# Optimization experiments

Hardware: AMD Instinct MI355X
Metric: run time of the kernel (lower is better)

The kernel has to match this reference:

```python
import jax, jax.numpy as jnp
import numpy as np

B, T, S, D, H, F = 8, 1024, 1024, 512, 8, 2048
LN_EPS = 1e-5


def _layernorm(x, g, b):
    m = jnp.mean(x, axis=-1, keepdims=True)
    v = jnp.mean((x - m) ** 2, axis=-1, keepdims=True)
    return (x - m) / jnp.sqrt(v + LN_EPS) * g + b


def setup_inputs() -> dict:
    key = jax.random.key(0)
    ks = jax.random.split(key, 32)
    p = lambda k, shape: jax.random.normal(k, shape, jnp.float32) * 0.02
    causal = jnp.where(jnp.triu(jnp.ones((T, T), dtype=bool), 1), -1e9, 0.0).astype(jnp.float32)
    return {
        "x": jax.random.normal(ks[0], (B, T, D), jnp.float32),
        "src_padding_mask": jnp.zeros((B, S, 1), jnp.float32),
        "src_subsq_mask": jnp.zeros((S, S), jnp.float32),  # unused by DecoderLayer math
        "tgt_padding_mask": jnp.zeros((B, T, 1), jnp.float32),
        "tgt_subsq_mask": causal,
        "mem_keys": jax.random.normal(ks[1], (B, S, D), jnp.float32),
        "mem_values": jax.random.normal(ks[2], (B, S, D), jnp.float32),
        # self-attention per-head params, stacked over heads (each head is full-D)
        "Wq_self": p(ks[3], (H, D, D)), "bq_self": p(ks[4], (H, D)),
        "Wk_self": p(ks[5], (H, D, D)), "bk_self": p(ks[6], (H, D)),
        "Wv_self": p(ks[7], (H, D, D)), "bv_self": p(ks[8], (H, D)),
        "Wo_self": p(ks[9], (H * D, D)), "bo_self": p(ks[10], (D,)),
        # memory (cross) attention: only Q per head; keys/values come from encoder
        "Wq_mem": p(ks[11], (H, D, D)), "bq_mem": p(ks[12], (H, D)),
        "Wo_mem": p(ks[13], (H * D, D)), "bo_mem": p(ks[14], (D,)),
        # FFN
        "W1": p(ks[15], (D, F)), "b1": p(ks[16], (F,)),
        "W2": p(ks[17], (F, D)), "b2": p(ks[18], (D,)),
        # LayerNorms
        "ln1_g": jnp.ones((D,), jnp.float32), "ln1_b": jnp.zeros((D,), jnp.float32),
        "ln2_g": jnp.ones((D,), jnp.float32), "ln2_b": jnp.zeros((D,), jnp.float32),
        "ln3_g": jnp.ones((D,), jnp.float32), "ln3_b": jnp.zeros((D,), jnp.float32),
    }


def reference(x, src_padding_mask, src_subsq_mask, tgt_padding_mask, tgt_subsq_mask,
              mem_keys, mem_values,
              Wq_self, bq_self, Wk_self, bk_self, Wv_self, bv_self, Wo_self, bo_self,
              Wq_mem, bq_mem, Wo_mem, bo_mem,
              W1, b1, W2, b2,
              ln1_g, ln1_b, ln2_g, ln2_b, ln3_g, ln3_b):
    b, t, d = x.shape
    h = Wq_self.shape[0]
    inv_sqrt_d = 1.0 / (d ** 0.5)

    # ---- multi-head self-attention (each head full d_model) ----
    q = jnp.einsum('btd,hde->bhte', x, Wq_self) + bq_self[None, :, None, :]
    k = jnp.einsum('btd,hde->bhte', x, Wk_self) + bk_self[None, :, None, :]
    v = jnp.einsum('btd,hde->bhte', x, Wv_self) + bv_self[None, :, None, :]
    att = jnp.einsum('bhte,bhse->bhts', q, k) * inv_sqrt_d
    att = att + tgt_padding_mask.transpose(0, 2, 1)[:, None, :, :]  # [B,1,1,T]
    att = att + tgt_subsq_mask[None, None, :, :]                     # [1,1,T,T]
    a = jax.nn.softmax(att, axis=-1)
    ho = jnp.einsum('bhts,bhse->bhte', a, v)
    cat = ho.transpose(0, 2, 1, 3).reshape(b, t, h * d)  # matches torch.cat head order
    sa = cat @ Wo_self + bo_self
    x1 = _layernorm(sa + x, ln1_g, ln1_b)  # dropout is identity at eval

    # ---- multi-head memory (cross) attention; keys/values shared across heads ----
    qm = jnp.einsum('btd,hde->bhte', x1, Wq_mem) + bq_mem[None, :, None, :]
    attm = jnp.einsum('bhte,bse->bhts', qm, mem_keys) * inv_sqrt_d
    attm = attm + src_padding_mask.transpose(0, 2, 1)[:, None, :, :]
    am = jax.nn.softmax(attm, axis=-1)
    hom = jnp.einsum('bhts,bse->bhte', am, mem_values)
    catm = hom.transpose(0, 2, 1, 3).reshape(b, t, h * d)
    ma = catm @ Wo_mem + bo_mem
    x2 = _layernorm(ma + x1, ln2_g, ln2_b)

    # ---- FFN ----
    ff = jax.nn.relu(x2 @ W1 + b1) @ W2 + b2
    out = _layernorm(ff + x2, ln3_g, ln3_b)
    return out
```

## Files before the change

### kernel.cpp

```cpp
#include <hip/hip_runtime.h>
#include <hip/hip_bf16.h>
#include <cstdint>

#define DEV __device__ __forceinline__

typedef __bf16 bf16_t;
typedef bf16_t bf16x8 __attribute__((ext_vector_type(8)));
typedef float  f32x4  __attribute__((ext_vector_type(4)));

static constexpr int B_ = 8, T_ = 1024, S_ = 1024, D_ = 512, H_ = 8, F_ = 2048;

typedef const __attribute__((address_space(1))) void* gas_ptr;
typedef __attribute__((address_space(3))) void* las_ptr;

DEV void gload_lds16(const void* g, void* l) {
  __builtin_amdgcn_global_load_lds((gas_ptr)g, (las_ptr)l, 16, 0, 0);
}

template<typename OutT, int EPI, int MI, int NI>
__global__ __launch_bounds__(256, (MI == 2 && NI == 2) ? 5 : 2) void gemm_bt(
    const bf16_t* __restrict__ A,  int64_t aH, int64_t aB, int lda,
    const bf16_t* __restrict__ BT, int64_t bH, int64_t bB, int ldb,
    OutT* __restrict__ C,          int64_t cH, int64_t cB, int ldo,
    int K, int ZB,
    const float* __restrict__ bias, int64_t biasH, int64_t biasB,
    float scale,
    const float* __restrict__ pad, int64_t padB,
    const float* __restrict__ subsq, int subsq_ld, int causal,
    int initC, int kcap)
{
  constexpr int BM = MI * 32;
  constexpr int BN = NI * 32;
  constexpr int BNT = NI * 32;

  const unsigned gx = gridDim.x, gy = gridDim.y;
  const unsigned nwg = gx * gy * gridDim.z;
  const unsigned orig = (blockIdx.z * gy + blockIdx.y) * gx + blockIdx.x;
  const unsigned q8 = nwg >> 3, r8 = nwg & 7;
  const unsigned xcd = orig & 7, cidx = orig >> 3;
  const unsigned swz = (xcd < r8 ? xcd * (q8 + 1)
                                 : r8 * (q8 + 1) + (xcd - r8) * q8) + cidx;
  const unsigned bz = swz / (gx * gy);
  const unsigned rm = swz - bz * gx * gy;
  const unsigned by = rm / gx;
  const unsigned bx = rm - by * gx;

  const int z  = bz;
  const int zh = z / ZB, zb = z - zh * ZB;
  A  += zh * aH + zb * aB;
  BT += zh * bH + zb * bB;
  C  += zh * cH + zb * cB;
  const int m0 = by * BM;
  const int n0 = bx * BNT;

  const bool skip = (EPI == 2) && causal && (n0 >= m0 + BM);
  if (skip && causal == 2) return;

  __shared__ __align__(16) bf16_t As[2][BM * 64];
  __shared__ __align__(16) bf16_t Bs[2][BNT * 64];

  const int tid  = threadIdx.x;
  const int lane = tid & 63;
  const int wr   = tid >> 7;
  const int wc   = (tid >> 6) & 1;

  f32x4 acc[MI][NI] = {};

  int Klim = K;
  if (kcap) { const int lim = m0 + BM; Klim = lim < K ? lim : K; }

  auto stage = [&](int buf, int kb) {
    #pragma unroll
    for (int i = 0; i < MI; ++i) {
      const int c = i * 256 + tid;
      const int row = c >> 3;
      const int col = (((c & 7) ^ (row & 7)) << 3);
      gload_lds16(A + (int64_t)(m0 + row) * lda + kb + col, &As[buf][c * 8]);
    }
    #pragma unroll
    for (int i = 0; i < NI; ++i) {
      const int c = i * 256 + tid;
      const int row = c >> 3;
      const int col = (((c & 7) ^ (row & 7)) << 3);
      gload_lds16(BT + (int64_t)(n0 + row) * ldb + kb + col, &Bs[buf][c * 8]);
    }
  };

  if (!skip) {
    const int NT = Klim >> 6;
    stage(0, 0);
    if (NT > 1) stage(1, 64);
    const int hi = lane >> 4, r7 = lane & 7;
    for (int t = 0; t < NT; ++t) {
      if (t + 1 < NT) {
        if constexpr (MI + NI == 4)      asm volatile("s_waitcnt vmcnt(4)" ::: "memory");
        else if constexpr (MI + NI == 6) asm volatile("s_waitcnt vmcnt(6)" ::: "memory");
        else                             asm volatile("s_waitcnt vmcnt(8)" ::: "memory");
      } else {
        asm volatile("s_waitcnt vmcnt(0)" ::: "memory");
      }
      __builtin_amdgcn_s_barrier();
      __builtin_amdgcn_sched_barrier(0);
      const int cur = t & 1;
      bf16x8 af[MI][2], bq[NI][2];
      #pragma unroll
      for (int ks = 0; ks < 2; ++ks) {
        #pragma unroll
        for (int i = 0; i < MI; ++i)
          af[i][ks] = *(const bf16x8*)&As[cur][(wr * (MI * 16) + i * 16 + (lane & 15)) * 64 + (((ks * 4 + hi) ^ r7) << 3)];
        #pragma unroll
        for (int i = 0; i < NI; ++i)
          bq[i][ks] = *(const bf16x8*)&Bs[cur][(wc * (NI * 16) + i * 16 + (lane & 15)) * 64 + (((ks * 4 + hi) ^ r7) << 3)];
      }
      asm volatile("s_waitcnt lgkmcnt(0)" ::: "memory");
      __builtin_amdgcn_sched_barrier(0);
      __builtin_amdgcn_s_barrier();
      if (t + 2 < NT) stage(cur, (t + 2) << 6);
      __builtin_amdgcn_sched_barrier(0);
      __builtin_amdgcn_s_setprio(1);
      #pragma unroll
      for (int ks = 0; ks < 2; ++ks)
        #pragma unroll
        for (int mi = 0; mi < MI; ++mi)
          #pragma unroll
          for (int ni = 0; ni < NI; ++ni)
            acc[mi][ni] = __builtin_amdgcn_mfma_f32_16x16x32_bf16(af[mi][ks], bq[ni][ks], acc[mi][ni], 0, 0, 0);
      __builtin_amdgcn_s_setprio(0);
    }
  }

  const float* bz_ = (EPI != 2 && bias) ? bias + zh * biasH + zb * biasB : nullptr;
  const float* pz  = (EPI == 2 && pad)  ? pad + zb * padB : nullptr;
  #pragma unroll
  for (int ni = 0; ni < NI; ++ni) {
    const int col = n0 + wc * (NI * 16) + ni * 16 + (lane & 15);
    const float badd = bz_ ? bz_[col] : 0.f;
    const float pv   = pz ? pz[col] : 0.f;
    #pragma unroll
    for (int mi = 0; mi < MI; ++mi) {
      const int rowb = m0 + wr * (MI * 16) + mi * 16 + ((lane >> 4) << 2);
      #pragma unroll
      for (int r = 0; r < 4; ++r) {
        const int row = rowb + r;
        const int64_t idx = (int64_t)row * ldo + col;
        float v = acc[mi][ni][r];
        if (EPI == 2) {
          if (skip) v = -1e9f;
          else {
            v = v * scale + pv;
            if (subsq) v += subsq[(int64_t)row * subsq_ld + col];
          }
        } else if (EPI == 3) {
          v += initC ? badd : (float)C[idx];
        } else {
          v += badd;
          if (EPI == 1) v = fmaxf(v, 0.f);
        }
        if constexpr (sizeof(OutT) == 2) C[idx] = (OutT)v;
        else                             C[idx] = v;
      }
    }
  }
  (void)BN;
}

template<int CAUSAL>
__global__ __launch_bounds__(256) void softmax1024b(bf16_t* __restrict__ P)
{
  const int64_t row = blockIdx.x;
  const int len = CAUSAL ? (int)(row % T_) + 1 : 1024;
  const int tid = threadIdx.x;
  const int j4 = tid << 2;
  float v0 = -3e38f, v1 = -3e38f, v2 = -3e38f, v3 = -3e38f;
  if (j4 < len) {
    union { bf16_t b[4]; uint2 u; } in;
    in.u = ((const uint2*)(P + row * 1024))[tid];
    v0 = (float)in.b[0];
    if (j4 + 1 < len) v1 = (float)in.b[1];
    if (j4 + 2 < len) v2 = (float)in.b[2];
    if (j4 + 3 < len) v3 = (float)in.b[3];
  }
  float m = fmaxf(fmaxf(v0, v1), fmaxf(v2, v3));
  #pragma unroll
  for (int off = 32; off; off >>= 1) m = fmaxf(m, __shfl_xor(m, off));
  __shared__ float red[8];
  if ((tid & 63) == 0) red[tid >> 6] = m;
  __syncthreads();
  m = fmaxf(fmaxf(red[0], red[1]), fmaxf(red[2], red[3]));
  const float e0 = (j4     < len) ? __expf(v0 - m) : 0.f;
  const float e1 = (j4 + 1 < len) ? __expf(v1 - m) : 0.f;
  const float e2 = (j4 + 2 < len) ? __expf(v2 - m) : 0.f;
  const float e3 = (j4 + 3 < len) ? __expf(v3 - m) : 0.f;
  float s = e0 + e1 + e2 + e3;
  #pragma unroll
  for (int off = 32; off; off >>= 1) s += __shfl_xor(s, off);
  if ((tid & 63) == 0) red[4 + (tid >> 6)] = s;
  __syncthreads();
  const float inv = 1.f / (red[4] + red[5] + red[6] + red[7]);
  const int lenc = CAUSAL ? ((len + 63) & ~63) : 1024;
  if (j4 < lenc) {
    union { bf16_t b[4]; uint2 u; } o;
    o.b[0] = (bf16_t)(e0 * inv); o.b[1] = (bf16_t)(e1 * inv);
    o.b[2] = (bf16_t)(e2 * inv); o.b[3] = (bf16_t)(e3 * inv);
    ((uint2*)(P + row * 1024))[tid] = o.u;
  }
}

__global__ __launch_bounds__(128) void add_ln512(
    const float* __restrict__ a, const float* __restrict__ r,
    const float* __restrict__ g, const float* __restrict__ be,
    float* __restrict__ yf, bf16_t* __restrict__ yb)
{
  const int64_t row = blockIdx.x;
  const int tid = threadIdx.x;
  const float4 va = ((const float4*)(a + row * 512))[tid];
  const float4 vr = ((const float4*)(r + row * 512))[tid];
  const float x0 = va.x + vr.x, x1 = va.y + vr.y, x2 = va.z + vr.z, x3 = va.w + vr.w;
  float s = x0 + x1 + x2 + x3;
  float q = x0 * x0 + x1 * x1 + x2 * x2 + x3 * x3;
  #pragma unroll
  for (int off = 32; off; off >>= 1) { s += __shfl_xor(s, off); q += __shfl_xor(q, off); }
  __shared__ float red[4];
  if ((tid & 63) == 0) { red[tid >> 6] = s; red[2 + (tid >> 6)] = q; }
  __syncthreads();
  s = red[0] + red[1]; q = red[2] + red[3];
  const float mean = s * (1.f / 512.f);
  const float var  = q * (1.f / 512.f) - mean * mean;
  const float rstd = rsqrtf(var + 1e-5f);
  const float4 g4 = ((const float4*)g)[tid];
  const float4 b4 = ((const float4*)be)[tid];
  const float y0 = (x0 - mean) * rstd * g4.x + b4.x;
  const float y1 = (x1 - mean) * rstd * g4.y + b4.y;
// ... 79 lines not shown
  float* outf = (float*)d_out;

  constexpr int64_t BTD = (int64_t)B_ * T_ * D_;
  constexpr int64_t BTS = (int64_t)B_ * T_ * S_;
  constexpr int64_t DD  = (int64_t)D_ * D_;
  const int M8 = B_ * T_;

  char* p = (char*)d_ws;
  auto alloc = [&](int64_t bytes) -> void* {
    char* r = p; p += (bytes + 255) & ~(int64_t)255; return (void*)r;
  };
  bf16_t* WTqkv = (bf16_t*)alloc(3 * H_ * DD * 2);
  bf16_t* WoT   = (bf16_t*)alloc((int64_t)D_ * H_ * D_ * 2);
  bf16_t* WqmT  = (bf16_t*)alloc(H_ * DD * 2);
  bf16_t* WomT  = (bf16_t*)alloc((int64_t)D_ * H_ * D_ * 2);
  bf16_t* W1T   = (bf16_t*)alloc((int64_t)F_ * D_ * 2);
  bf16_t* W2T   = (bf16_t*)alloc((int64_t)D_ * F_ * 2);
  float*  bqkv  = (float*)alloc(3 * H_ * D_ * 4);
  bf16_t* actb  = (bf16_t*)alloc(BTD * 2);
  bf16_t* mkb   = (bf16_t*)alloc(BTD * 2);
  bf16_t* mvT   = (bf16_t*)alloc(BTD * 2);
  float*  x1f   = (float*)alloc(BTD * 4);

  const int64_t remain = (int64_t)ws_size - (int64_t)(p - (char*)d_ws);
  const int64_t perG   = 3 * BTD * 2 + BTD * 2 + BTS * 2;
  const int64_t hoCat  = (int64_t)B_ * T_ * H_ * D_ * 2;
  int G = 0;
  for (int g = 8; g >= 1; g >>= 1)
    if (remain >= hoCat + (int64_t)g * perG + (4 << 20)) { G = g; break; }
  const int64_t needB = 3 * BTD * 2 + BTD * 2 + BTS * 2 + BTD * 2 + (1 << 20);
  if (G == 0 && remain < needB) return;

  const float scale = 1.0f / sqrtf((float)D_);
  dim3 blk(256);

  castf2b<<<dim3((unsigned)(BTD / 4 / 256)), blk, 0, stream>>>(x, actb, (int)(BTD / 4));
  castf2b<<<dim3((unsigned)(BTD / 4 / 256)), blk, 0, stream>>>(mk, mkb, (int)(BTD / 4));
  tcast<float><<<dim3(D_ / 32, S_ / 32, B_), blk, 0, stream>>>(mv, mvT, S_, D_);
  tcast<float><<<dim3(D_ / 32, D_ / 32, H_), blk, 0, stream>>>(Wq, WTqkv, D_, D_);
  tcast<float><<<dim3(D_ / 32, D_ / 32, H_), blk, 0, stream>>>(Wk, WTqkv + H_ * DD, D_, D_);
  tcast<float><<<dim3(D_ / 32, D_ / 32, H_), blk, 0, stream>>>(Wv, WTqkv + 2 * H_ * DD, D_, D_);
  tcast<float><<<dim3(D_ / 32, (H_ * D_) / 32, 1), blk, 0, stream>>>(Wo, WoT, H_ * D_, D_);
  tcast<float><<<dim3(D_ / 32, D_ / 32, H_), blk, 0, stream>>>(Wqm, WqmT, D_, D_);
  tcast<float><<<dim3(D_ / 32, (H_ * D_) / 32, 1), blk, 0, stream>>>(Wom, WomT, H_ * D_, D_);
  tcast<float><<<dim3(F_ / 32, D_ / 32, 1), blk, 0, stream>>>(W1, W1T, D_, F_);
  tcast<float><<<dim3(D_ / 32, F_ / 32, 1), blk, 0, stream>>>(W2, W2T, F_, D_);
  pack3<<<dim3((H_ * D_ + 255) / 256), blk, 0, stream>>>(bq, bk, bv, bqkv, H_ * D_);

  bf16_t* ffh = nullptr;

  if (G > 0) {
    bf16_t* hoAll = (bf16_t*)alloc(hoCat);
    bf16_t* qkv   = (bf16_t*)alloc(3 * G * BTD * 2);
    bf16_t* vt    = (bf16_t*)alloc((int64_t)G * BTD * 2);
    bf16_t* logit = (bf16_t*)alloc((int64_t)G * BTS * 2);
    ffh = qkv;

    for (int h0 = 0; h0 < H_; h0 += G) {
      gemm_bt<bf16_t, 0, 2, 2><<<dim3(D_ / 64, M8 / 64, 3 * G), blk, 0, stream>>>(
          actb, 0, 0, D_,
          WTqkv + (int64_t)h0 * DD, (int64_t)H_ * DD, DD, D_,
          qkv, (int64_t)G * BTD, BTD, D_,
          D_, G,
          bqkv + h0 * D_, (int64_t)H_ * D_, D_,
          1.f, nullptr, 0, nullptr, 0, 0, 0, 0);
      tcast<bf16_t><<<dim3(D_ / 32, T_ / 32, G * B_), blk, 0, stream>>>(
          qkv + (int64_t)2 * G * BTD, vt, T_, D_);
      gemm_bt<bf16_t, 2, 2, 2><<<dim3(S_ / 64, T_ / 64, G * B_), blk, 0, stream>>>(
          qkv, BTD, (int64_t)T_ * D_, D_,
          qkv + (int64_t)G * BTD, BTD, (int64_t)T_ * D_, D_,
          logit, BTS, (int64_t)T_ * S_, S_,
          D_, B_,
          nullptr, 0, 0,
          scale, tgt_pad, T_, tgt_sub, S_, 2, 0, 0);
      softmax1024b<1><<<dim3((unsigned)(G * B_ * T_)), blk, 0, stream>>>(logit);
      gemm_bt<bf16_t, 0, 2, 2><<<dim3(D_ / 64, T_ / 64, G * B_), blk, 0, stream>>>(
          logit, BTS, (int64_t)T_ * S_, S_,
          vt, (int64_t)B_ * D_ * T_, (int64_t)D_ * T_, T_,
          hoAll + (int64_t)h0 * D_, D_, (int64_t)T_ * H_ * D_, H_ * D_,
          S_, B_,
          nullptr, 0, 0, 1.f, nullptr, 0, nullptr, 0, 0, 0, 1);
    }
    gemm_bt<float, 0, 2, 2><<<dim3(D_ / 64, M8 / 64, 1), blk, 0, stream>>>(
        hoAll, 0, 0, H_ * D_, WoT, 0, 0, H_ * D_, outf, 0, 0, D_,
        H_ * D_, 1, bo, 0, 0, 1.f, nullptr, 0, nullptr, 0, 0, 0, 0);
    add_ln512<<<dim3(M8), dim3(128), 0, stream>>>(outf, x, g1, be1, x1f, actb);

    for (int h0 = 0; h0 < H_; h0 += G) {
      gemm_bt<bf16_t, 0, 2, 2><<<dim3(D_ / 64, M8 / 64, G), blk, 0, stream>>>(
          actb, 0, 0, D_,
          WqmT + (int64_t)h0 * DD, 0, DD, D_,
          qkv, 0, BTD, D_,
          D_, G,
          bqm + h0 * D_, 0, D_,
          1.f, nullptr, 0, nullptr, 0, 0, 0, 0);
      gemm_bt<bf16_t, 2, 2, 2><<<dim3(S_ / 64, T_ / 64, G * B_), blk, 0, stream>>>(
          qkv, BTD, (int64_t)T_ * D_, D_,
          mkb, 0, (int64_t)S_ * D_, D_,
          logit, BTS, (int64_t)T_ * S_, S_,
          D_, B_,
          nullptr, 0, 0,
          scale, src_pad, S_, nullptr, 0, 0, 0, 0);
      softmax1024b<0><<<dim3((unsigned)(G * B_ * T_)), blk, 0, stream>>>(logit);
      gemm_bt<bf16_t, 0, 2, 2><<<dim3(D_ / 64, T_ / 64, G * B_), blk, 0, stream>>>(
          logit, BTS, (int64_t)T_ * S_, S_,
          mvT, 0, (int64_t)D_ * S_, S_,
          hoAll + (int64_t)h0 * D_, D_, (int64_t)T_ * H_ * D_, H_ * D_,
          S_, B_,
          nullptr, 0, 0, 1.f, nullptr, 0, nullptr, 0, 0, 0, 0);
    }
    gemm_bt<float, 0, 2, 2><<<dim3(D_ / 64, M8 / 64, 1), blk, 0, stream>>>(
        hoAll, 0, 0, H_ * D_, WomT, 0, 0, H_ * D_, outf, 0, 0, D_,
        H_ * D_, 1, bom, 0, 0, 1.f, nullptr, 0, nullptr, 0, 0, 0, 0);
    add_ln512<<<dim3(M8), dim3(128), 0, stream>>>(outf, x1f, g2, be2, x1f, actb);
  } else {
    bf16_t* qkvH  = (bf16_t*)alloc(3 * BTD * 2);
    bf16_t* vtH   = (bf16_t*)alloc(BTD * 2);
    bf16_t* logit = (bf16_t*)alloc(BTS * 2);
    bf16_t* hoH   = (bf16_t*)alloc(BTD * 2);
    ffh = qkvH;

    for (int h = 0; h < H_; ++h) {
      gemm_bt<bf16_t, 0, 2, 2><<<dim3(D_ / 64, M8 / 64, 3), blk, 0, stream>>>(
          actb, 0, 0, D_,
          WTqkv + (int64_t)h * DD, (int64_t)H_ * DD, 0, D_,
          qkvH, BTD, 0, D_,
          D_, 1,
          bqkv + h * D_, (int64_t)H_ * D_, 0,
          1.f, nullptr, 0, nullptr, 0, 0, 0, 0);
      tcast<bf16_t><<<dim3(D_ / 32, T_ / 32, B_), blk, 0, stream>>>(
          qkvH + 2 * BTD, vtH, T_, D_);
      gemm_bt<bf16_t, 2, 2, 2><<<dim3(S_ / 64, T_ / 64, B_), blk, 0, stream>>>(
          qkvH, 0, (int64_t)T_ * D_, D_,
          qkvH + BTD, 0, (int64_t)T_ * D_, D_,
          logit, 0, (int64_t)T_ * S_, S_,
          D_, B_,
          nullptr, 0, 0,
          scale, tgt_pad, T_, tgt_sub, S_, 2, 0, 0);
      softmax1024b<1><<<dim3((unsigned)(B_ * T_)), blk, 0, stream>>>(logit);
      gemm_bt<bf16_t, 0, 2, 2><<<dim3(D_ / 64, T_ / 64, B_), blk, 0, stream>>>(
          logit, 0, (int64_t)T_ * S_, S_,
          vtH, 0, (int64_t)D_ * T_, T_,
          hoH, 0, (int64_t)T_ * D_, D_,
          S_, B_,
          nullptr, 0, 0, 1.f, nullptr, 0, nullptr, 0, 0, 0, 1);
      gemm_bt<float, 3, 2, 2><<<dim3(D_ / 64, M8 / 64, 1), blk, 0, stream>>>(
          hoH, 0, 0, D_,
          WoT + (int64_t)h * D_, 0, 0, H_ * D_,
          outf, 0, 0, D_,
          D_, 1,
          bo, 0, 0, 1.f, nullptr, 0, nullptr, 0, 0, (h == 0) ? 1 : 0, 0);
    }
    add_ln512<<<dim3(M8), dim3(128), 0, stream>>>(outf, x, g1, be1, x1f, actb);

    for (int h = 0; h < H_; ++h) {
      gemm_bt<bf16_t, 0, 2, 2><<<dim3(D_ / 64, M8 / 64, 1), blk, 0, stream>>>(
          actb, 0, 0, D_,
          WqmT + (int64_t)h * DD, 0, 0, D_,
          qkvH, 0, 0, D_,
          D_, 1,
          bqm + h * D_, 0, 0,
          1.f, nullptr, 0, nullptr, 0, 0, 0, 0);
      gemm_bt<bf16_t, 2, 2, 2><<<dim3(S_ / 64, T_ / 64, B_), blk, 0, stream>>>(
          qkvH, 0, (int64_t)T_ * D_, D_,
          mkb, 0, (int64_t)S_ * D_, D_,
          logit, 0, (int64_t)T_ * S_, S_,
          D_, B_,
          nullptr, 0, 0,
          scale, src_pad, S_, nullptr, 0, 0, 0, 0);
      softmax1024b<0><<<dim3((unsigned)(B_ * T_)), blk, 0, stream>>>(logit);
      gemm_bt<bf16_t, 0, 2, 2><<<dim3(D_ / 64, T_ / 64, B_), blk, 0, stream>>>(
          logit, 0, (int64_t)T_ * S_, S_,
          mvT, 0, (int64_t)D_ * S_, S_,
          hoH, 0, (int64_t)T_ * D_, D_,
          S_, B_,
          nullptr, 0, 0, 1.f, nullptr, 0, nullptr, 0, 0, 0, 0);
      gemm_bt<float, 3, 2, 2><<<dim3(D_ / 64, M8 / 64, 1), blk, 0, stream>>>(
          hoH, 0, 0, D_,
          WomT + (int64_t)h * D_, 0, 0, H_ * D_,
          outf, 0, 0, D_,
          D_, 1,
          bom, 0, 0, 1.f, nullptr, 0, nullptr, 0, 0, (h == 0) ? 1 : 0, 0);
    }
    add_ln512<<<dim3(M8), dim3(128), 0, stream>>>(outf, x1f, g2, be2, x1f, actb);
  }

  gemm_bt<bf16_t, 1, 2, 2><<<dim3(F_ / 64, M8 / 64, 1), blk, 0, stream>>>(
      actb, 0, 0, D_, W1T, 0, 0, D_, ffh, 0, 0, F_,
      D_, 1, b1, 0, 0, 1.f, nullptr, 0, nullptr, 0, 0, 0, 0);
  gemm_bt<float, 0, 2, 2><<<dim3(D_ / 64, M8 / 64, 1), blk, 0, stream>>>(
      ffh, 0, 0, F_, W2T, 0, 0, F_, outf, 0, 0, D_,
      F_, 1, b2, 0, 0, 1.f, nullptr, 0, nullptr, 0, 0, 0, 0);
  add_ln512<<<dim3(M8), dim3(128), 0, stream>>>(outf, x1f, g3, be3, outf, nullptr);

  (void)in_sizes; (void)n_in; (void)out_size;
}
```

Measured before the change: 1.146 ms.

## Add 256x256-tile 512-thread GEMM kernel for large attention and FFN GEMMs

Introduces a new gemm256 kernel with 256x256 output tiles, 8 waves, double-buffered LDS and s_setprio around the MFMA block. It is used for the batched QKV, logits, PV, cross-attention and W1 GEMMs in the grouped path. Output-projection and W2 GEMMs move from 64x64 to 64x128 tiles. The causal softmax zero-fill granularity now matches the tile size, and fully masked logit tiles are skipped outright. Larger tiles raise operand reuse and cut global/LDS traffic per FLOP, at the cost of fewer workgroups, higher register pressure and coarser causal skipping.

```diff
diff --git a/kernel.cpp b/kernel.cpp
--- a/kernel.cpp
+++ b/kernel.cpp
@@ -17,8 +17,151 @@
   __builtin_amdgcn_global_load_lds((gas_ptr)g, (las_ptr)l, 16, 0, 0);
 }
 
+DEV unsigned xcd_swizzle() {
+  const unsigned gx = gridDim.x, gy = gridDim.y;
+  const unsigned nwg = gx * gy * gridDim.z;
+  const unsigned orig = (blockIdx.z * gy + blockIdx.y) * gx + blockIdx.x;
+  const unsigned q8 = nwg >> 3, r8 = nwg & 7;
+  const unsigned xcd = orig & 7, cidx = orig >> 3;
+  return (xcd < r8 ? xcd * (q8 + 1) : r8 * (q8 + 1) + (xcd - r8) * q8) + cidx;
+}
+
+template<typename OutT, int EPI>
+__global__ __launch_bounds__(512, 2) void gemm256(
+    const bf16_t* __restrict__ A,  int64_t aH, int64_t aB, int lda,
+    const bf16_t* __restrict__ BT, int64_t bH, int64_t bB, int ldb,
+    OutT* __restrict__ C,          int64_t cH, int64_t cB, int ldo,
+    int K, int ZB,
+    const float* __restrict__ bias, int64_t biasH, int64_t biasB,
+    float scale,
+    const float* __restrict__ pad, int64_t padB,
+    const float* __restrict__ subsq, int subsq_ld, int causal,
+    int kcap)
+{
+  const unsigned gx = gridDim.x, gy = gridDim.y;
+  const unsigned swz = xcd_swizzle();
+  const unsigned bz = swz / (gx * gy);
+  const unsigned rm = swz - bz * gx * gy;
+  const unsigned by = rm / gx;
+  const unsigned bx = rm - by * gx;
+
+  const int z  = bz;
+  const int zh = z / ZB, zb = z - zh * ZB;
+  A  += zh * aH + zb * aB;
+  BT += zh * bH + zb * bB;
+  C  += zh * cH + zb * cB;
+  const int m0 = by << 8;
+  const int n0 = bx << 8;
+
+  const bool skip = (EPI == 2) && causal && (n0 >= m0 + 256);
+  if (skip) return;
+
+  __shared__ __align__(16) bf16_t As[2][256 * 64];
+  __shared__ __align__(16) bf16_t Bs[2][256 * 64];
+
+  const int tid  = threadIdx.x;
+  const int lane = tid & 63;
+  const int wid  = tid >> 6;
+  const int wr   = wid >> 2;
+  const int wc   = wid & 3;
+
+  f32x4 acc[8][4] = {};
+
+  int Klim = K;
+  if (kcap) { const int lim = m0 + 256; Klim = lim < K ? lim : K; }
+  const int NT = Klim >> 6;
+
+  auto stage = [&](int buf, int kb) {
+    #pragma unroll
+    for (int i = 0; i < 4; ++i) {
+      const int c = i * 512 + tid;
+      const int row = c >> 3;
+      const int col = (((c & 7) ^ (row & 7)) << 3);
+      gload_lds16(A + (int64_t)(m0 + row) * lda + kb + col, &As[buf][c * 8]);
+    }
+    #pragma unroll
+    for (int i = 0; i < 4; ++i) {
+      const int c = i * 512 + tid;
+      const int row = c >> 3;
+      const int col = (((c & 7) ^ (row & 7)) << 3);
+      gload_lds16(BT + (int64_t)(n0 + row) * ldb + kb + col, &Bs[buf][c * 8]);
+    }
+  };
+
+  stage(0, 0);
+  if (NT > 1) stage(1, 64);
+
+  const int hi = lane >> 4, l15 = lane & 15;
+  for (int t = 0; t < NT; ++t) {
+    if (t + 1 < NT) asm volatile("s_waitcnt vmcnt(8)" ::: "memory");
+    else            asm volatile("s_waitcnt vmcnt(0)" ::: "memory");
+    __builtin_amdgcn_s_barrier();
+    const int cur = t & 1;
+
+    bf16x8 bq[4][2];
+    #pragma unroll
+    for (int ks = 0; ks < 2; ++ks)
+      #pragma unroll
+      for (int ni = 0; ni < 4; ++ni) {
+        const int row = wc * 64 + ni * 16 + l15;
+        bq[ni][ks] = *(const bf16x8*)&Bs[cur][row * 64 + (((ks * 4 + hi) ^ (row & 7)) << 3)];
+      }
+    __builtin_amdgcn_s_setprio(1);
+    #pragma unroll
+    for (int mh = 0; mh < 2; ++mh) {
+      bf16x8 af[4][2];
+      #pragma unroll
+      for (int ks = 0; ks < 2; ++ks)
+        #pragma unroll
+        for (int mi = 0; mi < 4; ++mi) {
+          const int row = wr * 128 + (mh * 4 + mi) * 16 + l15;
+          af[mi][ks] = *(const bf16x8*)&As[cur][row * 64 + (((ks * 4 + hi) ^ (row & 7)) << 3)];
+        }
+      #pragma unroll
+      for (int ks = 0; ks < 2; ++ks)
+        #pragma unroll
+        for (int mi = 0; mi < 4; ++mi)
+          #pragma unroll
+          for (int ni = 0; ni < 4; ++ni)
+            acc[mh * 4 + mi][ni] = __builtin_amdgcn_mfma_f32_16x16x32_bf16(
+                af[mi][ks], bq[ni][ks], acc[mh * 4 + mi][ni], 0, 0, 0);
+    }
+    __builtin_amdgcn_s_setprio(0);
+    __builtin_amdgcn_s_barrier();
+    if (t + 2 < NT) stage(cur, (t + 2) << 6);
+  }
+
+  const float* bz_ = (EPI != 2 && bias) ? bias + zh * biasH + zb * biasB : nullptr;
+  const float* pz  = (EPI == 2 && pad)  ? pad + zb * padB : nullptr;
+  #pragma unroll
+  for (int ni = 0; ni < 4; ++ni) {
+    const int col = n0 + wc * 64 + ni * 16 + l15;
+    const float badd = bz_ ? bz_[col] : 0.f;
+    const float pv   = pz ? pz[col] : 0.f;
+    #pragma unroll
+    for (int mi = 0; mi < 8; ++mi) {
+      const int rowb = m0 + wr * 128 + mi * 16 + (hi << 2);
+      #pragma unroll
+      for (int r = 0; r < 4; ++r) {
+        const int row = rowb + r;
+        const int64_t idx = (int64_t)row * ldo + col;
+        float v = acc[mi][ni][r];
+        if (EPI == 2) {
+          v = v * scale + pv;
+          if (subsq) v += subsq[(int64_t)row * subsq_ld + col];
+        } else {
+          v += badd;
+          if (EPI == 1) v = fmaxf(v, 0.f);
+        }
+        if constexpr (sizeof(OutT) == 2) C[idx] = (OutT)v;
+        else                             C[idx] = v;
+      }
+    }
+  }
+}
+
 template<typename OutT, int EPI, int MI, int NI>
-__global__ __launch_bounds__(256, (MI == 2 && NI == 2) ? 5 : 2) void gemm_bt(
+__global__ __launch_bounds__(256, (MI == 2) ? 3 : 2) void gemm_bt(
     const bf16_t* __restrict__ A,  int64_t aH, int64_t aB, int lda,
     const bf16_t* __restrict__ BT, int64_t bH, int64_t bB, int ldb,
     OutT* __restrict__ C,          int64_t cH, int64_t cB, int ldo,
@@ -29,17 +172,11 @@
     const float* __restrict__ subsq, int subsq_ld, int causal,
     int initC, int kcap)
 {
-  constexpr int BM = MI * 32;
-  constexpr int BN = NI * 32;
+  constexpr int BM  = MI * 32;
   constexpr int BNT = NI * 32;
 
   const unsigned gx = gridDim.x, gy = gridDim.y;
-  const unsigned nwg = gx * gy * gridDim.z;
-  const unsigned orig = (blockIdx.z * gy + blockIdx.y) * gx + blockIdx.x;
-  const unsigned q8 = nwg >> 3, r8 = nwg & 7;
-  const unsigned xcd = orig & 7, cidx = orig >> 3;
-  const unsigned swz = (xcd < r8 ? xcd * (q8 + 1)
-                                 : r8 * (q8 + 1) + (xcd - r8) * q8) + cidx;
+  const unsigned swz = xcd_swizzle();
   const unsigned bz = swz / (gx * gy);
   const unsigned rm = swz - bz * gx * gy;
   const unsigned by = rm / gx;
@@ -93,9 +230,8 @@
     const int hi = lane >> 4, r7 = lane & 7;
     for (int t = 0; t < NT; ++t) {
       if (t + 1 < NT) {
-        if constexpr (MI + NI == 4)      asm volatile("s_waitcnt vmcnt(4)" ::: "memory");
-        else if constexpr (MI + NI == 6) asm volatile("s_waitcnt vmcnt(6)" ::: "memory");
-        else                             asm volatile("s_waitcnt vmcnt(8)" ::: "memory");
+        if constexpr (MI + NI == 6) asm volatile("s_waitcnt vmcnt(6)" ::: "memory");
+        else                        asm volatile("s_waitcnt vmcnt(4)" ::: "memory");
       } else {
         asm volatile("s_waitcnt vmcnt(0)" ::: "memory");
       }
@@ -161,10 +297,9 @@
       }
     }
   }
-  (void)BN;
-}
-
-template<int CAUSAL>
+}
+
+template<int CAUSAL, int ZF>
 __global__ __launch_bounds__(256) void softmax1024b(bf16_t* __restrict__ P)
 {
   const int64_t row = blockIdx.x;
@@ -197,7 +332,7 @@
   if ((tid & 63) == 0) red[4 + (tid >> 6)] = s;
   __syncthreads();
   const float inv = 1.f / (red[4] + red[5] + red[6] + red[7]);
-  const int lenc = CAUSAL ? ((len + 63) & ~63) : 1024;
+  const int lenc = CAUSAL ? ((len + ZF - 1) & ~(ZF - 1)) : 1024;
   if (j4 < lenc) {
     union { bf16_t b[4]; uint2 u; } o;
     o.b[0] = (bf16_t)(e0 * inv); o.b[1] = (bf16_t)(e1 * inv);
@@ -343,7 +478,7 @@
   if (G == 0 && remain < needB) return;
 
   const float scale = 1.0f / sqrtf((float)D_);
-  dim3 blk(256);
+  dim3 blk(256), blk5(512);
 
   castf2b<<<dim3((unsigned)(BTD / 4 / 256)), blk, 0, stream>>>(x, actb, (int)(BTD / 4));
   castf2b<<<dim3((unsigned)(BTD / 4 / 256)), blk, 0, stream>>>(mk, mkb, (int)(BTD / 4));
@@ -368,62 +503,66 @@
     ffh = qkv;
 
     for (int h0 = 0; h0 < H_; h0 += G) {
-      gemm_bt<bf16_t, 0, 2, 2><<<dim3(D_ / 64, M8 / 64, 3 * G), blk, 0, stream>>>(
+      gemm256<bf16_t, 0><<<dim3(D_ / 256, M8 / 256, 3 * G), blk5, 0, stream>>>(
           actb, 0, 0, D_,
           WTqkv + (int64_t)h0 * DD, (int64_t)H_ * DD, DD, D_,
           qkv, (int64_t)G * BTD, BTD, D_,
           D_, G,
           bqkv + h0 * D_, (int64_t)H_ * D_, D_,
-          1.f, nullptr, 0, nullptr, 0, 0, 0, 0);
+          1.f, nullptr, 0, nullptr, 0, 0, 0);
       tcast<bf16_t><<<dim3(D_ / 32, T_ / 32, G * B_), blk, 0, stream>>>(
           qkv + (int64_t)2 * G * BTD, vt, T_, D_);
-      gemm_bt<bf16_t, 2, 2, 2><<<dim3(S_ / 64, T_ / 64, G * B_), blk, 0, stream>>>(
+      gemm256<bf16_t, 2><<<dim3(S_ / 256, T_ / 256, G * B_), blk5, 0, stream>>>(
           qkv, BTD, (int64_t)T_ * D_, D_,
           qkv + (int64_t)G * BTD, BTD, (int64_t)T_ * D_, D_,
           logit, BTS, (int64_t)T_ * S_, S_,
           D_, B_,
           nullptr, 0, 0,
-          scale, tgt_pad, T_, tgt_sub, S_, 2, 0, 0);
-      softmax1024b<1><<<dim3((unsigned)(G * B_ * T_)), blk, 0, stream>>>(logit);
-      gemm_bt<bf16_t, 0, 2, 2><<<dim3(D_ / 64, T_ / 64, G * B_), blk, 0, stream>>>(
+          scale, tgt_pad, T_, tgt_sub, S_, 2, 0);
+      softmax1024b<1, 256><<<dim3((unsigned)(G * B_ * T_)), blk, 0, stream>>>(logit);
+      gemm256<bf16_t, 0><<<dim3(D_ / 256, T_ / 256, G * B_), blk5, 0, stream>>>(
           logit, BTS, (int64_t)T_ * S_, S_,
           vt, (int64_t)B_ * D_ * T_, (int64_t)D_ * T_, T_,
           hoAll + (int64_t)h0 * D_, D_, (int64_t)T_ * H_ * D_, H_ * D_,
           S_, B_,
-          nullptr, 0, 0, 1.f, nullptr, 0, nullptr, 0, 0, 0, 1);
-    }
-    gemm_bt<float, 0, 2, 2><<<dim3(D_ / 64, M8 / 64, 1), blk, 0, stream>>>(
+          nullptr, 0, 0, 1.f, nullptr, 0, nullptr, 0, 0, 1);
+    }
+    gemm_bt<float, 0, 2, 4><<<dim3(D_ / 128, M8 / 64, 1), blk, 0, stream>>>(
         hoAll, 0, 0, H_ * D_, WoT, 0, 0, H_ * D_, outf, 0, 0, D_,
         H_ * D_, 1, bo, 0, 0, 1.f, nullptr, 0, nullptr, 0, 0, 0, 0);
     add_ln512<<<dim3(M8), dim3(128), 0, stream>>>(outf, x, g1, be1, x1f, actb);
 
     for (int h0 = 0; h0 < H_; h0 += G) {
-      gemm_bt<bf16_t, 0, 2, 2><<<dim3(D_ / 64, M8 / 64, G), blk, 0, stream>>>(
+      gemm256<bf16_t, 0><<<dim3(D_ / 256, M8 / 256, G), blk5, 0, stream>>>(
           actb, 0, 0, D_,
           WqmT + (int64_t)h0 * DD, 0, DD, D_,
           qkv, 0, BTD, D_,
           D_, G,
           bqm + h0 * D_, 0, D_,
-          1.f, nullptr, 0, nullptr, 0, 0, 0, 0);
-      gemm_bt<bf16_t, 2, 2, 2><<<dim3(S_ / 64, T_ / 64, G * B_), blk, 0, stream>>>(
+          1.f, nullptr, 0, nullptr, 0, 0, 0);
+      gemm256<bf16_t, 2><<<dim3(S_ / 256, T_ / 256, G * B_), blk5, 0, stream>>>(
           qkv, BTD, (int64_t)T_ * D_, D_,
           mkb, 0, (int64_t)S_ * D_, D_,
           logit, BTS, (int64_t)T_ * S_, S_,
           D_, B_,
           nullptr, 0, 0,
-          scale, src_pad, S_, nullptr, 0, 0, 0, 0);
-      softmax1024b<0><<<dim3((unsigned)(G * B_ * T_)), blk, 0, stream>>>(logit);
-      gemm_bt<bf16_t, 0, 2, 2><<<dim3(D_ / 64, T_ / 64, G * B_), blk, 0, stream>>>(
+          scale, src_pad, S_, nullptr, 0, 0, 0);
+      softmax1024b<0, 64><<<dim3((unsigned)(G * B_ * T_)), blk, 0, stream>>>(logit);
+      gemm256<bf16_t, 0><<<dim3(D_ / 256, T_ / 256, G * B_), blk5, 0, stream>>>(
           logit, BTS, (int64_t)T_ * S_, S_,
           mvT, 0, (int64_t)D_ * S_, S_,
           hoAll + (int64_t)h0 * D_, D_, (int64_t)T_ * H_ * D_, H_ * D_,
           S_, B_,
-          nullptr, 0, 0, 1.f, nullptr, 0, nullptr, 0, 0, 0, 0);
-    }
-    gemm_bt<float, 0, 2, 2><<<dim3(D_ / 64, M8 / 64, 1), blk, 0, stream>>>(
+          nullptr, 0, 0, 1.f, nullptr, 0, nullptr, 0, 0, 0);
+    }
+    gemm_bt<float, 0, 2, 4><<<dim3(D_ / 128, M8 / 64, 1), blk, 0, stream>>>(
         hoAll, 0, 0, H_ * D_, WomT, 0, 0, H_ * D_, outf, 0, 0, D_,
         H_ * D_, 1, bom, 0, 0, 1.f, nullptr, 0, nullptr, 0, 0, 0, 0);
     add_ln512<<<dim3(M8), dim3(128), 0, stream>>>(outf, x1f, g2, be2, x1f, actb);
+
+    gemm256<bf16_t, 1><<<dim3(F_ / 256, M8 / 256, 1), blk5, 0, stream>>>(
+        actb, 0, 0, D_, W1T, 0, 0, D_, ffh, 0, 0, F_,
+        D_, 1, b1, 0, 0, 1.f, nullptr, 0, nullptr, 0, 0, 0);
   } else {
     bf16_t* qkvH  = (bf16_t*)alloc(3 * BTD * 2);
     bf16_t* vtH   = (bf16_t*)alloc(BTD * 2);
@@ -432,7 +571,7 @@
     ffh = qkvH;
 
     for (int h = 0; h < H_; ++h) {
-      gemm_bt<bf16_t, 0, 2, 2><<<dim3(D_ / 64, M8 / 64, 3), blk, 0, stream>>>(
+      gemm_bt<bf16_t, 0, 2, 4><<<dim3(D_ / 128, M8 / 64, 3), blk, 0, stream>>>(
           actb, 0, 0, D_,
           WTqkv + (int64_t)h * DD, (int64_t)H_ * DD, 0, D_,
           qkvH, BTD, 0, D_,
@@ -441,21 +580,21 @@
           1.f, nullptr, 0, nullptr, 0, 0, 0, 0);
       tcast<bf16_t><<<dim3(D_ / 32, T_ / 32, B_), blk, 0, stream>>>(
           qkvH + 2 * BTD, vtH, T_, D_);
-      gemm_bt<bf16_t, 2, 2, 2><<<dim3(S_ / 64, T_ / 64, B_), blk, 0, stream>>>(
+      gemm_bt<bf16_t, 2, 2, 4><<<dim3(S_ / 128, T_ / 64, B_), blk, 0, stream>>>(
           qkvH, 0, (int64_t)T_ * D_, D_,
           qkvH + BTD, 0, (int64_t)T_ * D_, D_,
           logit, 0, (int64_t)T_ * S_, S_,
           D_, B_,
           nullptr, 0, 0,
           scale, tgt_pad, T_, tgt_sub, S_, 2, 0, 0);
-      softmax1024b<1><<<dim3((unsigned)(B_ * T_)), blk, 0, stream>>>(logit);
-      gemm_bt<bf16_t, 0, 2, 2><<<dim3(D_ / 64, T_ / 64, B_), blk, 0, stream>>>(
+      softmax1024b<1, 64><<<dim3((unsigned)(B_ * T_)), blk, 0, stream>>>(logit);
+      gemm_bt<bf16_t, 0, 2, 4><<<dim3(D_ / 128, T_ / 64, B_), blk, 0, stream>>>(
           logit, 0, (int64_t)T_ * S_, S_,
           vtH, 0, (int64_t)D_ * T_, T_,
           hoH, 0, (int64_t)T_ * D_, D_,
           S_, B_,
           nullptr, 0, 0, 1.f, nullptr, 0, nullptr, 0, 0, 0, 1);
-      gemm_bt<float, 3, 2, 2><<<dim3(D_ / 64, M8 / 64, 1), blk, 0, stream>>>(
+      gemm_bt<float, 3, 2, 4><<<dim3(D_ / 128, M8 / 64, 1), blk, 0, stream>>>(
           hoH, 0, 0, D_,
           WoT + (int64_t)h * D_, 0, 0, H_ * D_,
           outf, 0, 0, D_,
@@ -465,28 +604,28 @@
     add_ln512<<<dim3(M8), dim3(128), 0, stream>>>(outf, x, g1, be1, x1f, actb);
 
     for (int h = 0; h < H_; ++h) {
-      gemm_bt<bf16_t, 0, 2, 2><<<dim3(D_ / 64, M8 / 64, 1), blk, 0, stream>>>(
+      gemm_bt<bf16_t, 0, 2, 4><<<dim3(D_ / 128, M8 / 64, 1), blk, 0, stream>>>(
           actb, 0, 0, D_,
           WqmT + (int64_t)h * DD, 0, 0, D_,
           qkvH, 0, 0, D_,
           D_, 1,
           bqm + h * D_, 0, 0,
           1.f, nullptr, 0, nullptr, 0, 0, 0, 0);
-      gemm_bt<bf16_t, 2, 2, 2><<<dim3(S_ / 64, T_ / 64, B_), blk, 0, stream>>>(
+      gemm_bt<bf16_t, 2, 2, 4><<<dim3(S_ / 128, T_ / 64, B_), blk, 0, stream>>>(
           qkvH, 0, (int64_t)T_ * D_, D_,
           mkb, 0, (int64_t)S_ * D_, D_,
           logit, 0, (int64_t)T_ * S_, S_,
           D_, B_,
           nullptr, 0, 0,
           scale, src_pad, S_, nullptr, 0, 0, 0, 0);
-      softmax1024b<0><<<dim3((unsigned)(B_ * T_)), blk, 0, stream>>>(logit);
-      gemm_bt<bf16_t, 0, 2, 2><<<dim3(D_ / 64, T_ / 64, B_), blk, 0, stream>>>(
+      softmax1024b<0, 64><<<dim3((unsigned)(B_ * T_)), blk, 0, stream>>>(logit);
+      gemm_bt<bf16_t, 0, 2, 4><<<dim3(D_ / 128, T_ / 64, B_), blk, 0, stream>>>(
           logit, 0, (int64_t)T_ * S_, S_,
           mvT, 0, (int64_t)D_ * S_, S_,
           hoH, 0, (int64_t)T_ * D_, D_,
           S_, B_,
           nullptr, 0, 0, 1.f, nullptr, 0, nullptr, 0, 0, 0, 0);
-      gemm_bt<float, 3, 2, 2><<<dim3(D_ / 64, M8 / 64, 1), blk, 0, stream>>>(
+      gemm_bt<float, 3, 2, 4><<<dim3(D_ / 128, M8 / 64, 1), blk, 0, stream>>>(
           hoH, 0, 0, D_,
           WomT + (int64_t)h * D_, 0, 0, H_ * D_,
           outf, 0, 0, D_,
@@ -494,12 +633,13 @@
           bom, 0, 0, 1.f, nullptr, 0, nullptr, 0, 0, (h == 0) ? 1 : 0, 0);
     }
     add_ln512<<<dim3(M8), dim3(128), 0, stream>>>(outf, x1f, g2, be2, x1f, actb);
-  }
-
-  gemm_bt<bf16_t, 1, 2, 2><<<dim3(F_ / 64, M8 / 64, 1), blk, 0, stream>>>(
-      actb, 0, 0, D_, W1T, 0, 0, D_, ffh, 0, 0, F_,
-      D_, 1, b1, 0, 0, 1.f, nullptr, 0, nullptr, 0, 0, 0, 0);
-  gemm_bt<float, 0, 2, 2><<<dim3(D_ / 64, M8 / 64, 1), blk, 0, stream>>>(
+
+    gemm_bt<bf16_t, 1, 2, 4><<<dim3(F_ / 128, M8 / 64, 1), blk, 0, stream>>>(
+        actb, 0, 0, D_, W1T, 0, 0, D_, ffh, 0, 0, F_,
+        D_, 1, b1, 0, 0, 1.f, nullptr, 0, nullptr, 0, 0, 0, 0);
+  }
+
+  gemm_bt<float, 0, 2, 4><<<dim3(D_ / 128, M8 / 64, 1), blk, 0, stream>>>(
       ffh, 0, 0, F_, W2T, 0, 0, F_, outf, 0, 0, D_,
       F_, 1, b2, 0, 0, 1.f, nullptr, 0, nullptr, 0, 0, 0, 0);
   add_ln512<<<dim3(M8), dim3(128), 0, stream>>>(outf, x1f, g3, be3, outf, nullptr);
```

New measurement: 1.343 ms. 17.2% more time.

## Triple-buffer GEMM LDS staging and widen tiles to 64x128

Applied to the files above, without the earlier changes.

The bf16 GEMM moves from double to triple LDS buffering, prefetching three K-slices ahead with wait counts that step down near the end of the loop. Every GEMM launch also switches from 64x64 to 64x128 output tiles, and the occupancy hint in launch_bounds drops from 5 to 2. The intent is to hide more global-load latency and raise operand reuse per block. In exchange each block uses much more LDS (about 73 KB) and gets fewer resident waves, and wider tiles skip fewer causal upper-triangle blocks. The explicit -1e9 write for skipped causal tiles is removed and the swizzle code is moved into a helper.

```diff
diff --git a/kernel.cpp b/kernel.cpp
--- a/kernel.cpp
+++ b/kernel.cpp
@@ -17,8 +17,17 @@
   __builtin_amdgcn_global_load_lds((gas_ptr)g, (las_ptr)l, 16, 0, 0);
 }
 
+DEV unsigned xcd_swizzle() {
+  const unsigned gx = gridDim.x, gy = gridDim.y;
+  const unsigned nwg = gx * gy * gridDim.z;
+  const unsigned orig = (blockIdx.z * gy + blockIdx.y) * gx + blockIdx.x;
+  const unsigned q8 = nwg >> 3, r8 = nwg & 7;
+  const unsigned xcd = orig & 7, cidx = orig >> 3;
+  return (xcd < r8 ? xcd * (q8 + 1) : r8 * (q8 + 1) + (xcd - r8) * q8) + cidx;
+}
+
 template<typename OutT, int EPI, int MI, int NI>
-__global__ __launch_bounds__(256, (MI == 2 && NI == 2) ? 5 : 2) void gemm_bt(
+__global__ __launch_bounds__(256, 2) void gemm_bt(
     const bf16_t* __restrict__ A,  int64_t aH, int64_t aB, int lda,
     const bf16_t* __restrict__ BT, int64_t bH, int64_t bB, int ldb,
     OutT* __restrict__ C,          int64_t cH, int64_t cB, int ldo,
@@ -29,17 +38,12 @@
     const float* __restrict__ subsq, int subsq_ld, int causal,
     int initC, int kcap)
 {
-  constexpr int BM = MI * 32;
-  constexpr int BN = NI * 32;
+  constexpr int BM  = MI * 32;
   constexpr int BNT = NI * 32;
+  constexpr int L   = MI + NI;
 
   const unsigned gx = gridDim.x, gy = gridDim.y;
-  const unsigned nwg = gx * gy * gridDim.z;
-  const unsigned orig = (blockIdx.z * gy + blockIdx.y) * gx + blockIdx.x;
-  const unsigned q8 = nwg >> 3, r8 = nwg & 7;
-  const unsigned xcd = orig & 7, cidx = orig >> 3;
-  const unsigned swz = (xcd < r8 ? xcd * (q8 + 1)
-                                 : r8 * (q8 + 1) + (xcd - r8) * q8) + cidx;
+  const unsigned swz = xcd_swizzle();
   const unsigned bz = swz / (gx * gy);
   const unsigned rm = swz - bz * gx * gy;
   const unsigned by = rm / gx;
@@ -56,8 +60,8 @@
   const bool skip = (EPI == 2) && causal && (n0 >= m0 + BM);
   if (skip && causal == 2) return;
 
-  __shared__ __align__(16) bf16_t As[2][BM * 64];
-  __shared__ __align__(16) bf16_t Bs[2][BNT * 64];
+  __shared__ __align__(16) bf16_t As[3][BM * 64];
+  __shared__ __align__(16) bf16_t Bs[3][BNT * 64];
 
   const int tid  = threadIdx.x;
   const int lane = tid & 63;
@@ -90,18 +94,27 @@
     const int NT = Klim >> 6;
     stage(0, 0);
     if (NT > 1) stage(1, 64);
+    if (NT > 2) stage(2, 128);
     const int hi = lane >> 4, r7 = lane & 7;
+    int cur = 0;
     for (int t = 0; t < NT; ++t) {
-      if (t + 1 < NT) {
-        if constexpr (MI + NI == 4)      asm volatile("s_waitcnt vmcnt(4)" ::: "memory");
-        else if constexpr (MI + NI == 6) asm volatile("s_waitcnt vmcnt(6)" ::: "memory");
-        else                             asm volatile("s_waitcnt vmcnt(8)" ::: "memory");
+      const int ahead0 = NT - 1 - t;
+      const int ahead = ahead0 > 2 ? 2 : ahead0;
+      if constexpr (L == 6) {
+        if (ahead == 2)      asm volatile("s_waitcnt vmcnt(12)" ::: "memory");
+        else if (ahead == 1) asm volatile("s_waitcnt vmcnt(6)"  ::: "memory");
+        else                 asm volatile("s_waitcnt vmcnt(0)"  ::: "memory");
+      } else if constexpr (L == 4) {
+        if (ahead == 2)      asm volatile("s_waitcnt vmcnt(8)"  ::: "memory");
+        else if (ahead == 1) asm volatile("s_waitcnt vmcnt(4)"  ::: "memory");
+        else                 asm volatile("s_waitcnt vmcnt(0)"  ::: "memory");
       } else {
-        asm volatile("s_waitcnt vmcnt(0)" ::: "memory");
+        if (ahead == 2)      asm volatile("s_waitcnt vmcnt(16)" ::: "memory");
+        else if (ahead == 1) asm volatile("s_waitcnt vmcnt(8)"  ::: "memory");
+        else                 asm volatile("s_waitcnt vmcnt(0)"  ::: "memory");
       }
       __builtin_amdgcn_s_barrier();
       __builtin_amdgcn_sched_barrier(0);
-      const int cur = t & 1;
       bf16x8 af[MI][2], bq[NI][2];
       #pragma unroll
       for (int ks = 0; ks < 2; ++ks) {
@@ -115,7 +128,7 @@
       asm volatile("s_waitcnt lgkmcnt(0)" ::: "memory");
       __builtin_amdgcn_sched_barrier(0);
       __builtin_amdgcn_s_barrier();
-      if (t + 2 < NT) stage(cur, (t + 2) << 6);
+      if (t + 3 < NT) stage(cur, (t + 3) << 6);
       __builtin_amdgcn_sched_barrier(0);
       __builtin_amdgcn_s_setprio(1);
       #pragma unroll
@@ -126,6 +139,7 @@
           for (int ni = 0; ni < NI; ++ni)
             acc[mi][ni] = __builtin_amdgcn_mfma_f32_16x16x32_bf16(af[mi][ks], bq[ni][ks], acc[mi][ni], 0, 0, 0);
       __builtin_amdgcn_s_setprio(0);
+      cur = (cur == 2) ? 0 : cur + 1;
     }
   }
 
@@ -145,11 +159,8 @@
         const int64_t idx = (int64_t)row * ldo + col;
         float v = acc[mi][ni][r];
         if (EPI == 2) {
-          if (skip) v = -1e9f;
-          else {
-            v = v * scale + pv;
-            if (subsq) v += subsq[(int64_t)row * subsq_ld + col];
-          }
+          v = v * scale + pv;
+          if (subsq) v += subsq[(int64_t)row * subsq_ld + col];
         } else if (EPI == 3) {
           v += initC ? badd : (float)C[idx];
         } else {
@@ -161,7 +172,6 @@
       }
     }
   }
-  (void)BN;
 }
 
 template<int CAUSAL>
@@ -368,7 +378,7 @@
     ffh = qkv;
 
     for (int h0 = 0; h0 < H_; h0 += G) {
-      gemm_bt<bf16_t, 0, 2, 2><<<dim3(D_ / 64, M8 / 64, 3 * G), blk, 0, stream>>>(
+      gemm_bt<bf16_t, 0, 2, 4><<<dim3(D_ / 128, M8 / 64, 3 * G), blk, 0, stream>>>(
           actb, 0, 0, D_,
           WTqkv + (int64_t)h0 * DD, (int64_t)H_ * DD, DD, D_,
           qkv, (int64_t)G * BTD, BTD, D_,
@@ -377,7 +387,7 @@
           1.f, nullptr, 0, nullptr, 0, 0, 0, 0);
       tcast<bf16_t><<<dim3(D_ / 32, T_ / 32, G * B_), blk, 0, stream>>>(
           qkv + (int64_t)2 * G * BTD, vt, T_, D_);
-      gemm_bt<bf16_t, 2, 2, 2><<<dim3(S_ / 64, T_ / 64, G * B_), blk, 0, stream>>>(
+      gemm_bt<bf16_t, 2, 2, 4><<<dim3(S_ / 128, T_ / 64, G * B_), blk, 0, stream>>>(
           qkv, BTD, (int64_t)T_ * D_, D_,
           qkv + (int64_t)G * BTD, BTD, (int64_t)T_ * D_, D_,
           logit, BTS, (int64_t)T_ * S_, S_,
@@ -385,27 +395,27 @@
           nullptr, 0, 0,
           scale, tgt_pad, T_, tgt_sub, S_, 2, 0, 0);
       softmax1024b<1><<<dim3((unsigned)(G * B_ * T_)), blk, 0, stream>>>(logit);
-      gemm_bt<bf16_t, 0, 2, 2><<<dim3(D_ / 64, T_ / 64, G * B_), blk, 0, stream>>>(
+      gemm_bt<bf16_t, 0, 2, 4><<<dim3(D_ / 128, T_ / 64, G * B_), blk, 0, stream>>>(
           logit, BTS, (int64_t)T_ * S_, S_,
           vt, (int64_t)B_ * D_ * T_, (int64_t)D_ * T_, T_,
           hoAll + (int64_t)h0 * D_, D_, (int64_t)T_ * H_ * D_, H_ * D_,
           S_, B_,
           nullptr, 0, 0, 1.f, nullptr, 0, nullptr, 0, 0, 0, 1);
     }
-    gemm_bt<float, 0, 2, 2><<<dim3(D_ / 64, M8 / 64, 1), blk, 0, stream>>>(
+    gemm_bt<float, 0, 2, 4><<<dim3(D_ / 128, M8 / 64, 1), blk, 0, stream>>>(
         hoAll, 0, 0, H_ * D_, WoT, 0, 0, H_ * D_, outf, 0, 0, D_,
         H_ * D_, 1, bo, 0, 0, 1.f, nullptr, 0, nullptr, 0, 0, 0, 0);
     add_ln512<<<dim3(M8), dim3(128), 0, stream>>>(outf, x, g1, be1, x1f, actb);
 
     for (int h0 = 0; h0 < H_; h0 += G) {
-      gemm_bt<bf16_t, 0, 2, 2><<<dim3(D_ / 64, M8 / 64, G), blk, 0, stream>>>(
+      gemm_bt<bf16_t, 0, 2, 4><<<dim3(D_ / 128, M8 / 64, G), blk, 0, stream>>>(
           actb, 0, 0, D_,
           WqmT + (int64_t)h0 * DD, 0, DD, D_,
           qkv, 0, BTD, D_,
           D_, G,
           bqm + h0 * D_, 0, D_,
           1.f, nullptr, 0, nullptr, 0, 0, 0, 0);
-      gemm_bt<bf16_t, 2, 2, 2><<<dim3(S_ / 64, T_ / 64, G * B_), blk, 0, stream>>>(
+      gemm_bt<bf16_t, 2, 2, 4><<<dim3(S_ / 128, T_ / 64, G * B_), blk, 0, stream>>>(
           qkv, BTD, (int64_t)T_ * D_, D_,
           mkb, 0, (int64_t)S_ * D_, D_,
           logit, BTS, (int64_t)T_ * S_, S_,
@@ -413,14 +423,14 @@
           nullptr, 0, 0,
           scale, src_pad, S_, nullptr, 0, 0, 0, 0);
       softmax1024b<0><<<dim3((unsigned)(G * B_ * T_)), blk, 0, stream>>>(logit);
-      gemm_bt<bf16_t, 0, 2, 2><<<dim3(D_ / 64, T_ / 64, G * B_), blk, 0, stream>>>(
+      gemm_bt<bf16_t, 0, 2, 4><<<dim3(D_ / 128, T_ / 64, G * B_), blk, 0, stream>>>(
           logit, BTS, (int64_t)T_ * S_, S_,
           mvT, 0, (int64_t)D_ * S_, S_,
           hoAll + (int64_t)h0 * D_, D_, (int64_t)T_ * H_ * D_, H_ * D_,
           S_, B_,
           nullptr, 0, 0, 1.f, nullptr, 0, nullptr, 0, 0, 0, 0);
     }
-    gemm_bt<float, 0, 2, 2><<<dim3(D_ / 64, M8 / 64, 1), blk, 0, stream>>>(
+    gemm_bt<float, 0, 2, 4><<<dim3(D_ / 128, M8 / 64, 1), blk, 0, stream>>>(
         hoAll, 0, 0, H_ * D_, WomT, 0, 0, H_ * D_, outf, 0, 0, D_,
         H_ * D_, 1, bom, 0, 0, 1.f, nullptr, 0, nullptr, 0, 0, 0, 0);
     add_ln512<<<dim3(M8), dim3(128), 0, stream>>>(outf, x1f, g2, be2, x1f, actb);
@@ -432,7 +442,7 @@
     ffh = qkvH;
 
     for (int h = 0; h < H_; ++h) {
-      gemm_bt<bf16_t, 0, 2, 2><<<dim3(D_ / 64, M8 / 64, 3), blk, 0, stream>>>(
+      gemm_bt<bf16_t, 0, 2, 4><<<dim3(D_ / 128, M8 / 64, 3), blk, 0, stream>>>(
           actb, 0, 0, D_,
           WTqkv + (int64_t)h * DD, (int64_t)H_ * DD, 0, D_,
           qkvH, BTD, 0, D_,
@@ -441,7 +451,7 @@
           1.f, nullptr, 0, nullptr, 0, 0, 0, 0);
       tcast<bf16_t><<<dim3(D_ / 32, T_ / 32, B_), blk, 0, stream>>>(
           qkvH + 2 * BTD, vtH, T_, D_);
-      gemm_bt<bf16_t, 2, 2, 2><<<dim3(S_ / 64, T_ / 64, B_), blk, 0, stream>>>(
+      gemm_bt<bf16_t, 2, 2, 4><<<dim3(S_ / 128, T_ / 64, B_), blk, 0, stream>>>(
           qkvH, 0, (int64_t)T_ * D_, D_,
           qkvH + BTD, 0, (int64_t)T_ * D_, D_,
           logit, 0, (int64_t)T_ * S_, S_,
@@ -449,13 +459,13 @@
           nullptr, 0, 0,
           scale, tgt_pad, T_, tgt_sub, S_, 2, 0, 0);
       softmax1024b<1><<<dim3((unsigned)(B_ * T_)), blk, 0, stream>>>(logit);
-      gemm_bt<bf16_t, 0, 2, 2><<<dim3(D_ / 64, T_ / 64, B_), blk, 0, stream>>>(
+      gemm_bt<bf16_t, 0, 2, 4><<<dim3(D_ / 128, T_ / 64, B_), blk, 0, stream>>>(
           logit, 0, (int64_t)T_ * S_, S_,
           vtH, 0, (int64_t)D_ * T_, T_,
           hoH, 0, (int64_t)T_ * D_, D_,
           S_, B_,
           nullptr, 0, 0, 1.f, nullptr, 0, nullptr, 0, 0, 0, 1);
-      gemm_bt<float, 3, 2, 2><<<dim3(D_ / 64, M8 / 64, 1), blk, 0, stream>>>(
+      gemm_bt<float, 3, 2, 4><<<dim3(D_ / 128, M8 / 64, 1), blk, 0, stream>>>(
           hoH, 0, 0, D_,
           WoT + (int64_t)h * D_, 0, 0, H_ * D_,
           outf, 0, 0, D_,
@@ -465,14 +475,14 @@
     add_ln512<<<dim3(M8), dim3(128), 0, stream>>>(outf, x, g1, be1, x1f, actb);
 
     for (int h = 0; h < H_; ++h) {
-      gemm_bt<bf16_t, 0, 2, 2><<<dim3(D_ / 64, M8 / 64, 1), blk, 0, stream>>>(
+      gemm_bt<bf16_t, 0, 2, 4><<<dim3(D_ / 128, M8 / 64, 1), blk, 0, stream>>>(
           actb, 0, 0, D_,
           WqmT + (int64_t)h * DD, 0, 0, D_,
           qkvH, 0, 0, D_,
           D_, 1,
           bqm + h * D_, 0, 0,
           1.f, nullptr, 0, nullptr, 0, 0, 0, 0);
-      gemm_bt<bf16_t, 2, 2, 2><<<dim3(S_ / 64, T_ / 64, B_), blk, 0, stream>>>(
+      gemm_bt<bf16_t, 2, 2, 4><<<dim3(S_ / 128, T_ / 64, B_), blk, 0, stream>>>(
           qkvH, 0, (int64_t)T_ * D_, D_,
           mkb, 0, (int64_t)S_ * D_, D_,
           logit, 0, (int64_t)T_ * S_, S_,
@@ -480,13 +490,13 @@
           nullptr, 0, 0,
           scale, src_pad, S_, nullptr, 0, 0, 0, 0);
       softmax1024b<0><<<dim3((unsigned)(B_ * T_)), blk, 0, stream>>>(logit);
-      gemm_bt<bf16_t, 0, 2, 2><<<dim3(D_ / 64, T_ / 64, B_), blk, 0, stream>>>(
+      gemm_bt<bf16_t, 0, 2, 4><<<dim3(D_ / 128, T_ / 64, B_), blk, 0, stream>>>(
           logit, 0, (int64_t)T_ * S_, S_,
           mvT, 0, (int64_t)D_ * S_, S_,
           hoH, 0, (int64_t)T_ * D_, D_,
           S_, B_,
           nullptr, 0, 0, 1.f, nullptr, 0, nullptr, 0, 0, 0, 0);
-      gemm_bt<float, 3, 2, 2><<<dim3(D_ / 64, M8 / 64, 1), blk, 0, stream>>>(
+      gemm_bt<float, 3, 2, 4><<<dim3(D_ / 128, M8 / 64, 1), blk, 0, stream>>>(
           hoH, 0, 0, D_,
           WomT + (int64_t)h * D_, 0, 0, H_ * D_,
           outf, 0, 0, D_,
@@ -496,10 +506,10 @@
     add_ln512<<<dim3(M8), dim3(128), 0, stream>>>(outf, x1f, g2, be2, x1f, actb);
   }
 
-  gemm_bt<bf16_t, 1, 2, 2><<<dim3(F_ / 64, M8 / 64, 1), blk, 0, stream>>>(
+  gemm_bt<bf16_t, 1, 2, 4><<<dim3(F_ / 128, M8 / 64, 1), blk, 0, stream>>>(
       actb, 0, 0, D_, W1T, 0, 0, D_, ffh, 0, 0, F_,
       D_, 1, b1, 0, 0, 1.f, nullptr, 0, nullptr, 0, 0, 0, 0);
-  gemm_bt<float, 0, 2, 2><<<dim3(D_ / 64, M8 / 64, 1), blk, 0, stream>>>(
+  gemm_bt<float, 0, 2, 4><<<dim3(D_ / 128, M8 / 64, 1), blk, 0, stream>>>(
       ffh, 0, 0, F_, W2T, 0, 0, F_, outf, 0, 0, D_,
       F_, 1, b2, 0, 0, 1.f, nullptr, 0, nullptr, 0, 0, 0, 0);
   add_ln512<<<dim3(M8), dim3(128), 0, stream>>>(outf, x1f, g3, be3, outf, nullptr);
```

Result: slower. 1.209 ms (+5.5%).
